# Kernel tuning notes

Hardware: AMD Instinct MI355X
Metric: run time of the kernel (lower is better)

## Reference

```python
import jax, jax.numpy as jnp
import numpy as np

N_NODES = 50000
N_EDGES = 400000
N_GRAPHS = 128
IN_DIM = 768
HID = 128
N_CLASSES = 11
BN_EPS = 1e-5


def _sage_conv(x, src, dst, Wl, bl, Wr):
    # PyG SAGEConv (aggr='mean'): out = lin_l(mean_{j->i} x_j) + lin_r(x_i)
    # messages flow src -> dst; nodes with no in-edges get a zero aggregate.
    n = x.shape[0]
    deg = jax.ops.segment_sum(jnp.ones_like(dst, x.dtype), dst, num_segments=n)
    agg = jax.ops.segment_sum(x[src], dst, num_segments=n)  # [N, d] gather+scatter
    agg = agg / jnp.maximum(deg, 1.0)[:, None]
    return agg @ Wl.T + bl + x @ Wr.T


def _batch_norm(x, gamma, beta):
    # training-mode BatchNorm1d: biased batch statistics over the node axis
    m = jnp.mean(x, axis=0)
    v = jnp.var(x, axis=0)
    return (x - m) * jax.lax.rsqrt(v + BN_EPS) * gamma + beta


def setup_inputs() -> dict:
    key = jax.random.key(0)
    ks = jax.random.split(key, 16)
    x = jax.random.normal(ks[0], (N_NODES, IN_DIM), dtype=jnp.float32)
    edge_index = jax.random.randint(ks[1], (2, N_EDGES), 0, N_NODES, dtype=jnp.int32)
    batch = jnp.sort(jax.random.randint(ks[2], (N_NODES,), 0, N_GRAPHS, dtype=jnp.int32))

    def lin_w(k, out_d, in_d):
        return jax.random.normal(k, (out_d, in_d), dtype=jnp.float32) * (1.0 / np.sqrt(in_d))

    params = {
        'W1l': lin_w(ks[3], HID, IN_DIM), 'b1': jnp.zeros((HID,), jnp.float32),
        'W1r': lin_w(ks[4], HID, IN_DIM),
        'g1': jnp.ones((HID,), jnp.float32), 'be1': jnp.zeros((HID,), jnp.float32),
        'W2l': lin_w(ks[5], HID, HID), 'b2': jnp.zeros((HID,), jnp.float32),
        'W2r': lin_w(ks[6], HID, HID),
        'g2': jnp.ones((HID,), jnp.float32), 'be2': jnp.zeros((HID,), jnp.float32),
        'W3l': lin_w(ks[7], HID, HID), 'b3': jnp.zeros((HID,), jnp.float32),
        'W3r': lin_w(ks[8], HID, HID),
        'g3': jnp.ones((HID,), jnp.float32), 'be3': jnp.zeros((HID,), jnp.float32),
        'Wlin': lin_w(ks[9], N_CLASSES, HID), 'blin': jnp.zeros((N_CLASSES,), jnp.float32),
    }
    return {'x': x, 'edge_index': edge_index, 'batch': batch, **params}


def reference(x, edge_index, batch,
              W1l, b1, W1r, g1, be1,
              W2l, b2, W2r, g2, be2,
              W3l, b3, W3r, g3, be3,
              Wlin, blin):
    src, dst = edge_index[0], edge_index[1]
    h = jax.nn.relu(_batch_norm(_sage_conv(x, src, dst, W1l, b1, W1r), g1, be1))
    h = jax.nn.relu(_batch_norm(_sage_conv(h, src, dst, W2l, b2, W2r), g2, be2))
    h = _batch_norm(_sage_conv(h, src, dst, W3l, b3, W3r), g3, be3)
    # global_max_pool over graph ids
    pooled = jax.ops.segment_max(h, batch, num_segments=N_GRAPHS)  # [G, HID]
    # dropout is identity at inference
    return pooled @ Wlin.T + blin  # [G, 11]
```

## Files before the change

### kernel.cpp

```cpp
#include <hip/hip_runtime.h>

#define N_NODESC 50000
#define N_EDGESC 400000
#define N_GRAPHSC 128
#define IN_DIMC 768
#define HIDC 128
#define NCLSC 11
#define BN_EPSC 1e-5f
#define NB_AGG 8
#define NREP 64
#define SCAN_NB ((N_NODESC + 255) / 256)

typedef __bf16 bf16_t;
typedef __bf16 bf16x8 __attribute__((ext_vector_type(8)));
typedef float f32x4 __attribute__((ext_vector_type(4)));

typedef __attribute__((address_space(1))) void glb_void;
typedef __attribute__((address_space(3))) void lds_void;

__device__ __forceinline__ void cp16(const void* g, void* l) {
    __builtin_amdgcn_global_load_lds((glb_void*)g, (lds_void*)l, 16, 0, 0);
}

__device__ __forceinline__ f32x4 mfma_16x16x32_bf16(bf16x8 a, bf16x8 b, f32x4 c) {
    return __builtin_amdgcn_mfma_f32_16x16x32_bf16(a, b, c, 0, 0, 0);
}

template<int MODE>
__global__ __launch_bounds__(256) void gemm_kernel(const void* __restrict__ Av,
                                                   const bf16_t* __restrict__ Wb,
                                                   const float* __restrict__ sc,
                                                   bf16_t* __restrict__ Cl,
                                                   bf16_t* __restrict__ Cr,
                                                   int M, int K)
{
    constexpr int ABYTES = (MODE == 0) ? 128 * 32 * 4 : 128 * 32 * 2;
    constexpr int AISS   = (MODE == 0) ? 4 : 2;
    constexpr int AESZ   = (MODE == 0) ? 4 : 2;
    __shared__ __align__(16) unsigned char smem[ABYTES + 128 * 32 * 2];
    unsigned char* Asm = smem;
    unsigned char* Bsm = smem + ABYTES;

    const int t    = threadIdx.x;
    const int m0   = blockIdx.x * 128;
    const int half = blockIdx.y;
    const int wid  = t >> 6;
    const int lane = t & 63;
    const int wm   = (wid >> 1) * 64;
    const int wn   = (wid & 1) * 64;
    const int l16  = lane & 15;
    const int quad = lane >> 4;

    const char* aSrc[AISS]; int aDst[AISS];
#pragma unroll
    for (int s = 0; s < AISS; s++) {
        int L = (s * 4 + wid) * 64 + lane;
        int r, c;
        if (MODE == 0) { r = L >> 3; c = (L & 7) ^ (r & 7); }
        else           { r = L >> 2; c = (L & 3) ^ ((r >> 1) & 3); }
        int row = m0 + r; if (row > M - 1) row = M - 1;
        aSrc[s] = (const char*)Av + ((size_t)row * K + (size_t)c * (16 / AESZ)) * AESZ;
        aDst[s] = (s * 4 + wid) * 1024;
    }
    const char* bSrc[2]; int bDst[2];
#pragma unroll
    for (int s = 0; s < 2; s++) {
        int L = (s * 4 + wid) * 64 + lane;
        int r = L >> 2;
        int c = (L & 3) ^ ((r >> 1) & 3);
        bSrc[s] = (const char*)(Wb + (size_t)(half * 128 + r) * K + c * 8);
        bDst[s] = (s * 4 + wid) * 1024;
    }

    int aOff[4][2], bOff[4];
#pragma unroll
    for (int i = 0; i < 4; i++) {
        int ra = wm + i * 16 + l16;
        if (MODE == 0) {
            aOff[i][0] = ra * 128 + (((2 * quad)     ^ (ra & 7)) * 16);
            aOff[i][1] = ra * 128 + (((2 * quad + 1) ^ (ra & 7)) * 16);
        } else {
            aOff[i][0] = ra * 64 + ((quad ^ ((ra >> 1) & 3)) * 16);
            aOff[i][1] = 0;
        }
        int rb = wn + i * 16 + l16;
        bOff[i] = rb * 64 + ((quad ^ ((rb >> 1) & 3)) * 16);
    }

    f32x4 acc[4][4] = {};

    for (int k0 = 0; k0 < K; k0 += 32) {
#pragma unroll
        for (int s = 0; s < AISS; s++)
            cp16(aSrc[s] + (size_t)k0 * AESZ, Asm + aDst[s]);
#pragma unroll
        for (int s = 0; s < 2; s++)
            cp16(bSrc[s] + (size_t)k0 * 2, Bsm + bDst[s]);
        __syncthreads();

        bf16x8 af[4], bfr[4];
        if (MODE == 0) {
#pragma unroll
            for (int i = 0; i < 4; i++) {
                float4 u0 = *(const float4*)(Asm + aOff[i][0]);
                float4 u1 = *(const float4*)(Asm + aOff[i][1]);
                af[i][0] = (bf16_t)u0.x; af[i][1] = (bf16_t)u0.y;
                af[i][2] = (bf16_t)u0.z; af[i][3] = (bf16_t)u0.w;
                af[i][4] = (bf16_t)u1.x; af[i][5] = (bf16_t)u1.y;
                af[i][6] = (bf16_t)u1.z; af[i][7] = (bf16_t)u1.w;
            }
        } else {
            const int ch0 = k0 + quad * 8;
            float4 s0 = *(const float4*)&sc[ch0];
            float4 s1 = *(const float4*)&sc[ch0 + 4];
            float4 h0 = *(const float4*)&sc[HIDC + ch0];
            float4 h1 = *(const float4*)&sc[HIDC + ch0 + 4];
            float ss[8] = {s0.x, s0.y, s0.z, s0.w, s1.x, s1.y, s1.z, s1.w};
            float hh[8] = {h0.x, h0.y, h0.z, h0.w, h1.x, h1.y, h1.z, h1.w};
#pragma unroll
            for (int i = 0; i < 4; i++) {
                bf16x8 raw = *(const bf16x8*)(Asm + aOff[i][0]);
#pragma unroll
                for (int e = 0; e < 8; e++)
                    af[i][e] = (bf16_t)fmaxf(fmaf((float)raw[e], ss[e], hh[e]), 0.0f);
            }
        }
#pragma unroll
        for (int j = 0; j < 4; j++)
            bfr[j] = *(const bf16x8*)(Bsm + bOff[j]);
#pragma unroll
        for (int i = 0; i < 4; i++)
#pragma unroll
            for (int j = 0; j < 4; j++)
                acc[i][j] = mfma_16x16x32_bf16(af[i], bfr[j], acc[i][j]);
        __syncthreads();
    }

    bf16_t* C = half ? Cr : Cl;
#pragma unroll
    for (int i = 0; i < 4; i++) {
        int rowb = m0 + wm + i * 16 + quad * 4;
#pragma unroll
        for (int j = 0; j < 4; j++) {
            int colh = wn + j * 16 + l16;
#pragma unroll
            for (int rr = 0; rr < 4; rr++) {
                int row = rowb + rr;
                if (row < M) C[(size_t)row * HIDC + colh] = (bf16_t)acc[i][j][rr];
            }
        }
    }
}

__global__ void wconv_kernel(const float* __restrict__ Wl, const float* __restrict__ Wr,
                             bf16_t* __restrict__ out, int KN)
{
    int i = blockIdx.x * blockDim.x + threadIdx.x;
    if (i < KN)           out[i] = (bf16_t)Wl[i];
    else if (i < 2 * KN)  out[i] = (bf16_t)Wr[i - KN];
}

__global__ void degi_kernel(const int* __restrict__ ei, int* __restrict__ degi) {
    int e = blockIdx.x * blockDim.x + threadIdx.x;
    if (e < N_EDGESC) atomicAdd(&degi[ei[N_EDGESC + e]], 1);
}

__global__ __launch_bounds__(256) void scan1_kernel(const int* __restrict__ degi,
                                                    int* __restrict__ local,
                                                    int* __restrict__ partials)
{
    __shared__ int tmp[256];
    const int t = threadIdx.x;
    const int i = blockIdx.x * 256 + t;
    int v = (i < N_NODESC) ? degi[i] : 0;
    tmp[t] = v;
    __syncthreads();
    for (int off = 1; off < 256; off <<= 1) {
        int u = (t >= off) ? tmp[t - off] : 0;
        __syncthreads();
        tmp[t] += u;
        __syncthreads();
    }
    if (i < N_NODESC) local[i] = tmp[t] - v;
    if (t == 255) partials[blockIdx.x] = tmp[255];
}

__global__ __launch_bounds__(256) void scan2_kernel(int* __restrict__ partials)
{
    __shared__ int tmp[256];
    const int t = threadIdx.x;
    int v = (t < SCAN_NB) ? partials[t] : 0;
    tmp[t] = v;
    __syncthreads();
    for (int off = 1; off < 256; off <<= 1) {
        int u = (t >= off) ? tmp[t - off] : 0;
        __syncthreads();
        tmp[t] += u;
        __syncthreads();
    }
    if (t < SCAN_NB) partials[t] = tmp[t] - v;
}

__global__ __launch_bounds__(256) void scan3_kernel(const int* __restrict__ local,
                                                    const int* __restrict__ partials,
                                                    int* __restrict__ rowptr,
                                                    int* __restrict__ cursor)
{
    const int i = blockIdx.x * 256 + threadIdx.x;
    if (i < N_NODESC) {
        int r = local[i] + partials[blockIdx.x];
        rowptr[i] = r;
        cursor[i] = r;
    }
    if (i == 0) rowptr[N_NODESC] = N_EDGESC;
}

__global__ void fill_kernel(const int* __restrict__ ei, int* __restrict__ cursor,
                            int* __restrict__ col) {
    int e = blockIdx.x * blockDim.x + threadIdx.x;
    if (e >= N_EDGESC) return;
    int d = ei[N_EDGESC + e];
    int pos = atomicAdd(&cursor[d], 1);
    col[pos] = ei[e];
}

__global__ __launch_bounds__(128) void agg_combine_kernel(const int* __restrict__ rowptr,
                                                          const int* __restrict__ col,
                                                          const bf16_t* __restrict__ Plb,
                                                          const bf16_t* __restrict__ Prb,
                                                          const float* __restrict__ bias,
                                                          bf16_t* __restrict__ Hb,
                                                          float* __restrict__ stats, int M)
{
    const int c = threadIdx.x;
    const float b = bias[c];
    float s = 0.f, s2 = 0.f;
    const int n0 = blockIdx.x * NB_AGG;
    for (int rr = 0; rr < NB_AGG; rr++) {
        int n = n0 + rr;
        if (n >= M) break;
        int lo = rowptr[n], hi = rowptr[n + 1];
        float a = 0.f;
        for (int e = lo; e < hi; e += 8) {
            int rem = hi - e;
            int idx[8];
#pragma unroll
            for (int j = 0; j < 8; j++) {
                int ee = e + j; if (ee > hi - 1) ee = hi - 1;
                idx[j] = col[ee];
            }
            float v[8];
#pragma unroll
            for (int j = 0; j < 8; j++)
                v[j] = (float)Plb[(size_t)idx[j] * HIDC + c];
#pragma unroll
            for (int j = 0; j < 8; j++)
                if (j < rem) a += v[j];
        }
        int d = hi - lo;
        float inv = 1.0f / (float)(d > 0 ? d : 1);
        float pre = fmaf(a, inv, b) + (float)Prb[(size_t)n * HIDC + c];
        Hb[(size_t)n * HIDC + c] = (bf16_t)pre;
        s += pre; s2 += pre * pre;
    }
    const int rep = blockIdx.x & (NREP - 1);
    atomicAdd(&stats[rep * 256 + c], s);
    atomicAdd(&stats[rep * 256 + HIDC + c], s2);
}

__global__ __launch_bounds__(128) void finalize_kernel(const float* __restrict__ stats,
                                                       const float* __restrict__ g,
                                                       const float* __restrict__ be,
                                                       float* __restrict__ sc, int M)
{
    int c = threadIdx.x;
    float sum = 0.f, sumsq = 0.f;
    for (int r = 0; r < NREP; r++) {
        sum   += stats[r * 256 + c];
        sumsq += stats[r * 256 + HIDC + c];
    }
    float invM = 1.0f / (float)M;
    float mean = sum * invM;
    float var  = sumsq * invM - mean * mean;
    float s = rsqrtf(var + BN_EPSC) * g[c];
    sc[c] = s;
    sc[HIDC + c] = be[c] - mean * s;
}

__global__ __launch_bounds__(128) void pool_kernel(const bf16_t* __restrict__ Hb,
                                                   const float* __restrict__ sc,
                                                   const int* __restrict__ batch,
                                                   float* __restrict__ pooled, int M)
{
    int gph = blockIdx.x;
    int c   = threadIdx.x;
    float s = sc[c], h = sc[HIDC + c];
    int lo = 0, hi = M;
    while (lo < hi) { int m = (lo + hi) >> 1; if (batch[m] < gph) lo = m + 1; else hi = m; }
    int lo2 = lo, hi2 = M;
    while (lo2 < hi2) { int m = (lo2 + hi2) >> 1; if (batch[m] < gph + 1) lo2 = m + 1; else hi2 = m; }
    float mx = -INFINITY;
    for (int rr = lo; rr < lo2; rr++)
        mx = fmaxf(mx, fmaf((float)Hb[(size_t)rr * HIDC + c], s, h));
    pooled[gph * HIDC + c] = mx;
}

__global__ __launch_bounds__(128) void final_kernel(const float* __restrict__ pooled,
                                                    const float* __restrict__ W,
                                                    const float* __restrict__ bl,
                                                    float* __restrict__ out)
{
    __shared__ float sp[HIDC];
    int gph = blockIdx.x;
    int t   = threadIdx.x;
    sp[t] = pooled[gph * HIDC + t];
    __syncthreads();
    if (t < NCLSC) {
        float acc = bl[t];
        for (int c = 0; c < HIDC; c++) acc += sp[c] * W[t * HIDC + c];
        out[gph * NCLSC + t] = acc;
    }
}

extern "C" void kernel_launch(void* const* d_in, const int* in_sizes, int n_in,
                              void* d_out, int out_size, void* d_ws, size_t ws_size,
                              hipStream_t stream)
{
    const float* x     = (const float*)d_in[0];
    const int*   ei    = (const int*)d_in[1];
    const int*   batch = (const int*)d_in[2];
    const float* W1l = (const float*)d_in[3];
    const float* b1  = (const float*)d_in[4];
    const float* W1r = (const float*)d_in[5];
    const float* g1  = (const float*)d_in[6];
    const float* be1 = (const float*)d_in[7];
    const float* W2l = (const float*)d_in[8];
    const float* b2  = (const float*)d_in[9];
    const float* W2r = (const float*)d_in[10];
    const float* g2  = (const float*)d_in[11];
    const float* be2 = (const float*)d_in[12];
    const float* W3l = (const float*)d_in[13];
    const float* b3  = (const float*)d_in[14];
    const float* W3r = (const float*)d_in[15];
    const float* g3  = (const float*)d_in[16];
    const float* be3 = (const float*)d_in[17];
    const float* Wlin = (const float*)d_in[18];
    const float* blin = (const float*)d_in[19];

    const int M = N_NODESC;

    char* w = (char*)d_ws;
    bf16_t* Plb  = (bf16_t*)w;  w += (size_t)M * HIDC * 2;
    bf16_t* Prb  = (bf16_t*)w;  w += (size_t)M * HIDC * 2;
    bf16_t* Hb   = (bf16_t*)w;  w += (size_t)M * HIDC * 2;
    bf16_t* Wb1  = (bf16_t*)w;  w += (size_t)256 * IN_DIMC * 2;
    bf16_t* Wb2  = (bf16_t*)w;  w += (size_t)256 * HIDC * 2;
    bf16_t* Wb3  = (bf16_t*)w;  w += (size_t)256 * HIDC * 2;
    int*   rowptr= (int*)w;     w += (size_t)(M + 16) * 4;
    int*   col   = (int*)w;     w += (size_t)N_EDGESC * 4;
    int*   cursor= (int*)w;     w += (size_t)M * 4;
    int*   degi  = (int*)w;     w += (size_t)M * 4;
    int*   slocal= (int*)w;     w += (size_t)M * 4;
    int*   spart = (int*)w;     w += 256 * 4;
    float* stats = (float*)w;   w += (size_t)NREP * 256 * 4;
    float* sc    = (float*)w;   w += 256 * 4;
    float* pooled= (float*)w;   w += (size_t)N_GRAPHSC * HIDC * 4;

    const dim3 gemm_grid((M + 127) / 128, 2);
    const int agg_blocks = (M + NB_AGG - 1) / NB_AGG;
    const size_t stats_bytes = (size_t)NREP * 256 * 4;

    wconv_kernel<<<(2 * 128 * IN_DIMC + 255) / 256, 256, 0, stream>>>(W1l, W1r, Wb1, 128 * IN_DIMC);
    wconv_kernel<<<(2 * 128 * HIDC + 255) / 256, 256, 0, stream>>>(W2l, W2r, Wb2, 128 * HIDC);
    wconv_kernel<<<(2 * 128 * HIDC + 255) / 256, 256, 0, stream>>>(W3l, W3r, Wb3, 128 * HIDC);

    hipMemsetAsync(degi, 0, (size_t)M * 4, stream);
    degi_kernel<<<(N_EDGESC + 255) / 256, 256, 0, stream>>>(ei, degi);
    scan1_kernel<<<SCAN_NB, 256, 0, stream>>>(degi, slocal, spart);
    scan2_kernel<<<1, 256, 0, stream>>>(spart);
    scan3_kernel<<<SCAN_NB, 256, 0, stream>>>(slocal, spart, rowptr, cursor);
    fill_kernel<<<(N_EDGESC + 255) / 256, 256, 0, stream>>>(ei, cursor, col);

    gemm_kernel<0><<<gemm_grid, 256, 0, stream>>>(x, Wb1, nullptr, Plb, Prb, M, IN_DIMC);
    hipMemsetAsync(stats, 0, stats_bytes, stream);
    agg_combine_kernel<<<agg_blocks, 128, 0, stream>>>(rowptr, col, Plb, Prb, b1, Hb, stats, M);
    finalize_kernel<<<1, 128, 0, stream>>>(stats, g1, be1, sc, M);

    gemm_kernel<1><<<gemm_grid, 256, 0, stream>>>(Hb, Wb2, sc, Plb, Prb, M, HIDC);
    hipMemsetAsync(stats, 0, stats_bytes, stream);
    agg_combine_kernel<<<agg_blocks, 128, 0, stream>>>(rowptr, col, Plb, Prb, b2, Hb, stats, M);
    finalize_kernel<<<1, 128, 0, stream>>>(stats, g2, be2, sc, M);

    gemm_kernel<1><<<gemm_grid, 256, 0, stream>>>(Hb, Wb3, sc, Plb, Prb, M, HIDC);
    hipMemsetAsync(stats, 0, stats_bytes, stream);
    agg_combine_kernel<<<agg_blocks, 128, 0, stream>>>(rowptr, col, Plb, Prb, b3, Hb, stats, M);
    finalize_kernel<<<1, 128, 0, stream>>>(stats, g3, be3, sc, M);

    pool_kernel<<<N_GRAPHSC, 128, 0, stream>>>(Hb, sc, batch, pooled, M);
    final_kernel<<<N_GRAPHSC, 128, 0, stream>>>(pooled, Wlin, blin, (float*)d_out);
}
```

Before: 584.3 us.

## Double-buffer GEMM K-loop, shrink M tile, vectorize aggregation to bf16x2

The GEMM now double-buffers its A and B LDS tiles with async global-to-LDS copies and explicit vmcnt waits, so the next K slice loads while MFMAs run on the current one. The M tile drops from 128 to 64 rows to launch more blocks, K becomes a template constant, and the BN scale/shift is staged in LDS. The aggregation kernel now has each lane handle two channels with bf16x2 loads, with two waves each covering half the nodes. The hand-written waitcnt counts and barriers add fragility, and the smaller tile reloads the B tile more often.

```diff
diff --git a/kernel.cpp b/kernel.cpp
--- a/kernel.cpp
+++ b/kernel.cpp
@@ -12,6 +12,7 @@
 #define SCAN_NB ((N_NODESC + 255) / 256)
 
 typedef __bf16 bf16_t;
+typedef __bf16 bf16x2 __attribute__((ext_vector_type(2)));
 typedef __bf16 bf16x8 __attribute__((ext_vector_type(8)));
 typedef float f32x4 __attribute__((ext_vector_type(4)));
 
@@ -26,27 +27,30 @@
     return __builtin_amdgcn_mfma_f32_16x16x32_bf16(a, b, c, 0, 0, 0);
 }
 
-template<int MODE>
+template<int MODE, int KC>
 __global__ __launch_bounds__(256) void gemm_kernel(const void* __restrict__ Av,
                                                    const bf16_t* __restrict__ Wb,
                                                    const float* __restrict__ sc,
                                                    bf16_t* __restrict__ Cl,
                                                    bf16_t* __restrict__ Cr,
-                                                   int M, int K)
-{
-    constexpr int ABYTES = (MODE == 0) ? 128 * 32 * 4 : 128 * 32 * 2;
-    constexpr int AISS   = (MODE == 0) ? 4 : 2;
-    constexpr int AESZ   = (MODE == 0) ? 4 : 2;
-    __shared__ __align__(16) unsigned char smem[ABYTES + 128 * 32 * 2];
+                                                   int M)
+{
+    constexpr int NK   = KC / 32;
+    constexpr int AESZ = (MODE == 0) ? 4 : 2;
+    constexpr int ASZ  = 64 * 32 * AESZ;
+    constexpr int BSZ  = 128 * 32 * 2;
+    constexpr int AISS = (MODE == 0) ? 2 : 1;
+    __shared__ __align__(16) unsigned char smem[2 * ASZ + 2 * BSZ + ((MODE == 1) ? 1024 : 16)];
     unsigned char* Asm = smem;
-    unsigned char* Bsm = smem + ABYTES;
+    unsigned char* Bsm = smem + 2 * ASZ;
+    float* scS = (float*)(smem + 2 * ASZ + 2 * BSZ);
 
     const int t    = threadIdx.x;
-    const int m0   = blockIdx.x * 128;
+    const int m0   = blockIdx.x * 64;
     const int half = blockIdx.y;
     const int wid  = t >> 6;
     const int lane = t & 63;
-    const int wm   = (wid >> 1) * 64;
+    const int wm   = (wid >> 1) * 32;
     const int wn   = (wid & 1) * 64;
     const int l16  = lane & 15;
     const int quad = lane >> 4;
@@ -59,7 +63,7 @@
         if (MODE == 0) { r = L >> 3; c = (L & 7) ^ (r & 7); }
         else           { r = L >> 2; c = (L & 3) ^ ((r >> 1) & 3); }
         int row = m0 + r; if (row > M - 1) row = M - 1;
-        aSrc[s] = (const char*)Av + ((size_t)row * K + (size_t)c * (16 / AESZ)) * AESZ;
+        aSrc[s] = (const char*)Av + ((size_t)row * KC + (size_t)c * (16 / AESZ)) * AESZ;
         aDst[s] = (s * 4 + wid) * 1024;
     }
     const char* bSrc[2]; int bDst[2];
@@ -68,13 +72,13 @@
         int L = (s * 4 + wid) * 64 + lane;
         int r = L >> 2;
         int c = (L & 3) ^ ((r >> 1) & 3);
-        bSrc[s] = (const char*)(Wb + (size_t)(half * 128 + r) * K + c * 8);
+        bSrc[s] = (const char*)(Wb + (size_t)(half * 128 + r) * KC + c * 8);
         bDst[s] = (s * 4 + wid) * 1024;
     }
 
-    int aOff[4][2], bOff[4];
-#pragma unroll
-    for (int i = 0; i < 4; i++) {
+    int aOff[2][2], bOff[4];
+#pragma unroll
+    for (int i = 0; i < 2; i++) {
         int ra = wm + i * 16 + l16;
         if (MODE == 0) {
             aOff[i][0] = ra * 128 + (((2 * quad)     ^ (ra & 7)) * 16);
@@ -83,43 +87,66 @@
             aOff[i][0] = ra * 64 + ((quad ^ ((ra >> 1) & 3)) * 16);
             aOff[i][1] = 0;
         }
-        int rb = wn + i * 16 + l16;
-        bOff[i] = rb * 64 + ((quad ^ ((rb >> 1) & 3)) * 16);
-    }
-
-    f32x4 acc[4][4] = {};
-
-    for (int k0 = 0; k0 < K; k0 += 32) {
-#pragma unroll
-        for (int s = 0; s < AISS; s++)
-            cp16(aSrc[s] + (size_t)k0 * AESZ, Asm + aDst[s]);
-#pragma unroll
-        for (int s = 0; s < 2; s++)
-            cp16(bSrc[s] + (size_t)k0 * 2, Bsm + bDst[s]);
+    }
+#pragma unroll
+    for (int j = 0; j < 4; j++) {
+        int rb = wn + j * 16 + l16;
+        bOff[j] = rb * 64 + ((quad ^ ((rb >> 1) & 3)) * 16);
+    }
+
+    if (MODE == 1) {
+        scS[t] = sc[t];
         __syncthreads();
-
-        bf16x8 af[4], bfr[4];
+    }
+
+#pragma unroll
+    for (int s = 0; s < AISS; s++) cp16(aSrc[s], Asm + aDst[s]);
+#pragma unroll
+    for (int s = 0; s < 2; s++)    cp16(bSrc[s], Bsm + bDst[s]);
+
+    f32x4 acc[2][4] = {};
+
+    for (int it = 0; it < NK; ++it) {
+        const int cur = it & 1;
+        if (it + 1 < NK) {
+            const int nxt = 1 - cur;
+            const size_t kb = (size_t)(it + 1) * 32;
+#pragma unroll
+            for (int s = 0; s < AISS; s++)
+                cp16(aSrc[s] + kb * AESZ, Asm + nxt * ASZ + aDst[s]);
+#pragma unroll
+            for (int s = 0; s < 2; s++)
+                cp16(bSrc[s] + kb * 2, Bsm + nxt * BSZ + bDst[s]);
+            if (MODE == 0) asm volatile("s_waitcnt vmcnt(4)" ::: "memory");
+            else           asm volatile("s_waitcnt vmcnt(3)" ::: "memory");
+        } else {
+            asm volatile("s_waitcnt vmcnt(0)" ::: "memory");
+        }
+        asm volatile("s_barrier" ::: "memory");
+
+        const unsigned char* Ab = Asm + cur * ASZ;
+        const unsigned char* Bb = Bsm + cur * BSZ;
+        bf16x8 af[2], bfr[4];
         if (MODE == 0) {
 #pragma unroll
-            for (int i = 0; i < 4; i++) {
-                float4 u0 = *(const float4*)(Asm + aOff[i][0]);
-                float4 u1 = *(const float4*)(Asm + aOff[i][1]);
+            for (int i = 0; i < 2; i++) {
+                float4 u0 = *(const float4*)(Ab + aOff[i][0]);
+                float4 u1 = *(const float4*)(Ab + aOff[i][1]);
                 af[i][0] = (bf16_t)u0.x; af[i][1] = (bf16_t)u0.y;
                 af[i][2] = (bf16_t)u0.z; af[i][3] = (bf16_t)u0.w;
                 af[i][4] = (bf16_t)u1.x; af[i][5] = (bf16_t)u1.y;
                 af[i][6] = (bf16_t)u1.z; af[i][7] = (bf16_t)u1.w;
             }
         } else {
-            const int ch0 = k0 + quad * 8;
-            float4 s0 = *(const float4*)&sc[ch0];
-            float4 s1 = *(const float4*)&sc[ch0 + 4];
-            float4 h0 = *(const float4*)&sc[HIDC + ch0];
-            float4 h1 = *(const float4*)&sc[HIDC + ch0 + 4];
+            float4 s0 = *(const float4*)&scS[it * 32 + quad * 8];
+            float4 s1 = *(const float4*)&scS[it * 32 + quad * 8 + 4];
+            float4 h0 = *(const float4*)&scS[HIDC + it * 32 + quad * 8];
+            float4 h1 = *(const float4*)&scS[HIDC + it * 32 + quad * 8 + 4];
             float ss[8] = {s0.x, s0.y, s0.z, s0.w, s1.x, s1.y, s1.z, s1.w};
             float hh[8] = {h0.x, h0.y, h0.z, h0.w, h1.x, h1.y, h1.z, h1.w};
 #pragma unroll
-            for (int i = 0; i < 4; i++) {
-                bf16x8 raw = *(const bf16x8*)(Asm + aOff[i][0]);
+            for (int i = 0; i < 2; i++) {
+                bf16x8 raw = *(const bf16x8*)(Ab + aOff[i][0]);
 #pragma unroll
                 for (int e = 0; e < 8; e++)
                     af[i][e] = (bf16_t)fmaxf(fmaf((float)raw[e], ss[e], hh[e]), 0.0f);
@@ -127,18 +154,19 @@
         }
 #pragma unroll
         for (int j = 0; j < 4; j++)
-            bfr[j] = *(const bf16x8*)(Bsm + bOff[j]);
-#pragma unroll
-        for (int i = 0; i < 4; i++)
+            bfr[j] = *(const bf16x8*)(Bb + bOff[j]);
+#pragma unroll
+        for (int i = 0; i < 2; i++)
 #pragma unroll
             for (int j = 0; j < 4; j++)
                 acc[i][j] = mfma_16x16x32_bf16(af[i], bfr[j], acc[i][j]);
-        __syncthreads();
+
+        asm volatile("s_barrier" ::: "memory");
     }
 
     bf16_t* C = half ? Cr : Cl;
 #pragma unroll
-    for (int i = 0; i < 4; i++) {
+    for (int i = 0; i < 2; i++) {
         int rowb = m0 + wm + i * 16 + quad * 4;
 #pragma unroll
         for (int j = 0; j < 4; j++) {
@@ -232,15 +260,17 @@
                                                           bf16_t* __restrict__ Hb,
                                                           float* __restrict__ stats, int M)
 {
-    const int c = threadIdx.x;
-    const float b = bias[c];
-    float s = 0.f, s2 = 0.f;
-    const int n0 = blockIdx.x * NB_AGG;
-    for (int rr = 0; rr < NB_AGG; rr++) {
+    const int lane = threadIdx.x & 63;
+    const int wv   = threadIdx.x >> 6;
+    const int c0   = lane * 2;
+    const float b0 = bias[c0], b1 = bias[c0 + 1];
+    float s0 = 0.f, s1 = 0.f, q0 = 0.f, q1 = 0.f;
+    const int n0 = blockIdx.x * NB_AGG + wv * (NB_AGG / 2);
+    for (int rr = 0; rr < NB_AGG / 2; rr++) {
         int n = n0 + rr;
         if (n >= M) break;
         int lo = rowptr[n], hi = rowptr[n + 1];
-        float a = 0.f;
+        float a0 = 0.f, a1 = 0.f;
         for (int e = lo; e < hi; e += 8) {
             int rem = hi - e;
             int idx[8];
@@ -249,23 +279,28 @@
                 int ee = e + j; if (ee > hi - 1) ee = hi - 1;
                 idx[j] = col[ee];
             }
-            float v[8];
+            bf16x2 v[8];
 #pragma unroll
             for (int j = 0; j < 8; j++)
-                v[j] = (float)Plb[(size_t)idx[j] * HIDC + c];
+                v[j] = *(const bf16x2*)&Plb[(size_t)idx[j] * HIDC + c0];
 #pragma unroll
             for (int j = 0; j < 8; j++)
-                if (j < rem) a += v[j];
+                if (j < rem) { a0 += (float)v[j][0]; a1 += (float)v[j][1]; }
         }
         int d = hi - lo;
         float inv = 1.0f / (float)(d > 0 ? d : 1);
-        float pre = fmaf(a, inv, b) + (float)Prb[(size_t)n * HIDC + c];
-        Hb[(size_t)n * HIDC + c] = (bf16_t)pre;
-        s += pre; s2 += pre * pre;
-    }
-    const int rep = blockIdx.x & (NREP - 1);
-    atomicAdd(&stats[rep * 256 + c], s);
-    atomicAdd(&stats[rep * 256 + HIDC + c], s2);
+        bf16x2 pr = *(const bf16x2*)&Prb[(size_t)n * HIDC + c0];
+        float pre0 = fmaf(a0, inv, b0) + (float)pr[0];
+        float pre1 = fmaf(a1, inv, b1) + (float)pr[1];
+        bf16x2 hv; hv[0] = (bf16_t)pre0; hv[1] = (bf16_t)pre1;
+        *(bf16x2*)&Hb[(size_t)n * HIDC + c0] = hv;
+        s0 += pre0; s1 += pre1; q0 += pre0 * pre0; q1 += pre1 * pre1;
+    }
+    const int rep = (blockIdx.x * 2 + wv) & (NREP - 1);
+    atomicAdd(&stats[rep * 256 + c0], s0);
+    atomicAdd(&stats[rep * 256 + c0 + 1], s1);
+    atomicAdd(&stats[rep * 256 + HIDC + c0], q0);
+    atomicAdd(&stats[rep * 256 + HIDC + c0 + 1], q1);
 }
 
 __global__ __launch_bounds__(128) void finalize_kernel(const float* __restrict__ stats,
@@ -366,7 +401,7 @@
     float* sc    = (float*)w;   w += 256 * 4;
     float* pooled= (float*)w;   w += (size_t)N_GRAPHSC * HIDC * 4;
 
-    const dim3 gemm_grid((M + 127) / 128, 2);
+    const dim3 gemm_grid((M + 63) / 64, 2);
     const int agg_blocks = (M + NB_AGG - 1) / NB_AGG;
     const size_t stats_bytes = (size_t)NREP * 256 * 4;
 
@@ -381,17 +416,17 @@
     scan3_kernel<<<SCAN_NB, 256, 0, stream>>>(slocal, spart, rowptr, cursor);
     fill_kernel<<<(N_EDGESC + 255) / 256, 256, 0, stream>>>(ei, cursor, col);
 
-    gemm_kernel<0><<<gemm_grid, 256, 0, stream>>>(x, Wb1, nullptr, Plb, Prb, M, IN_DIMC);
+    gemm_kernel<0, IN_DIMC><<<gemm_grid, 256, 0, stream>>>(x, Wb1, nullptr, Plb, Prb, M);
     hipMemsetAsync(stats, 0, stats_bytes, stream);
     agg_combine_kernel<<<agg_blocks, 128, 0, stream>>>(rowptr, col, Plb, Prb, b1, Hb, stats, M);
     finalize_kernel<<<1, 128, 0, stream>>>(stats, g1, be1, sc, M);
 
-    gemm_kernel<1><<<gemm_grid, 256, 0, stream>>>(Hb, Wb2, sc, Plb, Prb, M, HIDC);
+    gemm_kernel<1, HIDC><<<gemm_grid, 256, 0, stream>>>(Hb, Wb2, sc, Plb, Prb, M);
     hipMemsetAsync(stats, 0, stats_bytes, stream);
     agg_combine_kernel<<<agg_blocks, 128, 0, stream>>>(rowptr, col, Plb, Prb, b2, Hb, stats, M);
     finalize_kernel<<<1, 128, 0, stream>>>(stats, g2, be2, sc, M);
 
-    gemm_kernel<1><<<gemm_grid, 256, 0, stream>>>(Hb, Wb3, sc, Plb, Prb, M, HIDC);
+    gemm_kernel<1, HIDC><<<gemm_grid, 256, 0, stream>>>(Hb, Wb3, sc, Plb, Prb, M);
     hipMemsetAsync(stats, 0, stats_bytes, stream);
     agg_combine_kernel<<<agg_blocks, 128, 0, stream>>>(rowptr, col, Plb, Prb, b3, Hb, stats, M);
     finalize_kernel<<<1, 128, 0, stream>>>(stats, g3, be3, sc, M);
```

New measurement: 590.5 us. No clear change (+1.1%).
